# Kernel optimization log

Hardware: AMD Instinct MI355X
Metric: run time of the kernel (lower is better)

Reference implementation:

```python
import jax, jax.numpy as jnp
import numpy as np

HIDDEN = 1024
BATCH = 32
SRC_LEN = 2048
NEG_BIG = -1e10


def setup_inputs() -> dict:
    key = jax.random.key(0)
    k1, k2, k3, k4, k5, k6 = jax.random.split(key, 6)
    s = 1.0 / np.sqrt(2 * HIDDEN)
    return {
        "decoder_hidden": jax.random.normal(k1, (BATCH, HIDDEN), dtype=jnp.float32),
        "encoder_outputs": jax.random.normal(k2, (BATCH, SRC_LEN, HIDDEN), dtype=jnp.float32),
        "mask": jax.random.randint(k3, (BATCH, SRC_LEN), 0, 2, dtype=jnp.int32),
        # attn: Linear(2H -> H). Store as (2H, H) so x @ W matches torch x @ W.T
        "attn_W": jax.random.uniform(k4, (2 * HIDDEN, HIDDEN), jnp.float32, -s, s),
        "attn_b": jax.random.uniform(k5, (HIDDEN,), jnp.float32, -s, s),
        # v: Linear(H -> 1, bias=False), stored as (H,)
        "v_w": jax.random.uniform(k6, (HIDDEN,), jnp.float32, -1.0 / np.sqrt(HIDDEN), 1.0 / np.sqrt(HIDDEN)),
    }


def reference(decoder_hidden, encoder_outputs, mask, attn_W, attn_b, v_w):
    # Split the concat-linear: [dec, enc] @ W == dec @ W_dec + enc @ W_enc (same math, no big concat)
    W_dec, W_enc = attn_W[:HIDDEN], attn_W[HIDDEN:]
    dec_proj = decoder_hidden @ W_dec + attn_b            # (B, H)
    enc_proj = jnp.einsum("bsh,hk->bsk", encoder_outputs, W_enc)  # (B, S, H)
    energy = jnp.tanh(dec_proj[:, None, :] + enc_proj)    # (B, S, H)
    attention = jnp.einsum("bsh,h->bs", energy, v_w)      # (B, S)
    attention = jnp.where(mask == 0, NEG_BIG, attention)
    attention_weights = jax.nn.softmax(attention, axis=1)  # (B, S)
    context = jnp.einsum("bs,bsh->bh", attention_weights, encoder_outputs)  # (B, H)
    return attention_weights, context
```

## Files before the change

### kernel.cpp

```cpp
#include <hip/hip_runtime.h>
#include <hip/hip_bf16.h>
#include <math.h>

#define HIDDEN 1024
#define BATCH 32
#define SRC_LEN 2048
#define NROWS (BATCH * SRC_LEN)
#define NEG_BIG -10000000000.0f

typedef __attribute__((ext_vector_type(8))) short bf16x8;
typedef __attribute__((ext_vector_type(4))) float f32x4;
typedef __attribute__((ext_vector_type(4))) unsigned uint32x4;

static __device__ __forceinline__ unsigned short f2bf(float f) {
  unsigned u = __float_as_uint(f);
  u = u + 0x7fffu + ((u >> 16) & 1u);
  return (unsigned short)(u >> 16);
}

static __device__ __forceinline__ unsigned cvtpk(float lo, float hi) {
  unsigned r;
  asm("v_cvt_pk_bf16_f32 %0, %1, %2" : "=v"(r) : "v"(lo), "v"(hi));
  return r;
}

static __device__ __forceinline__ void gload16(const void* g, void* l) {
  __builtin_amdgcn_global_load_lds(
      reinterpret_cast<const __attribute__((address_space(1))) unsigned*>(
          reinterpret_cast<unsigned long long>(g)),
      reinterpret_cast<__attribute__((address_space(3))) unsigned*>(
          reinterpret_cast<unsigned long long>(l)),
      16, 0, 0);
}

__global__ __launch_bounds__(256) void k_wt(
    const float* __restrict__ W, unsigned short* __restrict__ WT) {
  __shared__ float ts[64][65];
  const int hy = blockIdx.y * 64, nx = blockIdx.x * 64;
  const int tid = threadIdx.x;
#pragma unroll
  for (int i = 0; i < 16; ++i) {
    int idx = tid + i * 256, r = idx >> 6, c = idx & 63;
    ts[r][c] = W[(HIDDEN + hy + r) * HIDDEN + nx + c];
  }
  __syncthreads();
#pragma unroll
  for (int i = 0; i < 16; ++i) {
    int idx = tid + i * 256, rn = idx >> 6, ch = idx & 63;
    WT[(nx + rn) * HIDDEN + hy + ch] = f2bf(ts[ch][rn]);
  }
}

__global__ __launch_bounds__(256) void k_dec_part(
    const float* __restrict__ dh, const float* __restrict__ W,
    float* __restrict__ decpart) {
  const int kl = threadIdx.x & 63;
  const int bq = threadIdx.x >> 6;
  const int k = blockIdx.x * 64 + kl;
  const int h0 = blockIdx.y * 64;
  __shared__ float dh_s[64][33];
#pragma unroll
  for (int i = 0; i < 8; ++i) {
    int idx = threadIdx.x + i * 256;
    int b = idx >> 6, hh = idx & 63;
    dh_s[hh][b] = dh[b * HIDDEN + h0 + hh];
  }
  __syncthreads();
  float acc[8] = {0.f, 0.f, 0.f, 0.f, 0.f, 0.f, 0.f, 0.f};
#pragma unroll
  for (int hh = 0; hh < 64; ++hh) {
    float w = W[(h0 + hh) * HIDDEN + k];
#pragma unroll
    for (int bb = 0; bb < 8; ++bb) acc[bb] += dh_s[hh][bq * 8 + bb] * w;
  }
#pragma unroll
  for (int bb = 0; bb < 8; ++bb)
    decpart[blockIdx.y * (BATCH * HIDDEN) + (bq * 8 + bb) * HIDDEN + k] = acc[bb];
}

__global__ __launch_bounds__(256) void k_dec_reduce(
    const float* __restrict__ decpart, const float* __restrict__ bias,
    float* __restrict__ out) {
  int e = blockIdx.x * 256 + threadIdx.x;
  float s = bias[e & (HIDDEN - 1)];
#pragma unroll
  for (int hc = 0; hc < 16; ++hc) s += decpart[hc * (BATCH * HIDDEN) + e];
  out[e] = s;
}

#define BM 256
#define BN 256
#define BK 64
#define NT (HIDDEN / BK)

__global__ __launch_bounds__(512, 2) void k_energy_mfma(
    const float* __restrict__ enc, const unsigned short* __restrict__ WT,
    const float* __restrict__ dec_proj, const float* __restrict__ v_w,
    float* __restrict__ part) {
  __shared__ unsigned short As[2][BM * BK];
  __shared__ unsigned short Bs[2][BN * BK];
  __shared__ float red[4][BM];

  const int tid = threadIdx.x;
  const int lane = tid & 63;
  const int wid = tid >> 6;
  const int wm = wid >> 2;
  const int wn = wid & 3;
  const int l16 = lane & 15;
  const int kg = lane >> 4;

  const int bid = blockIdx.x;
  const int l = (bid & 7) * 128 + (bid >> 3);
  const int n0 = (l & 3) * BN;
  const int row0 = (l >> 2) * BM;
  const int b = row0 >> 11;

  f32x4 acc[8][4];
#pragma unroll
  for (int m = 0; m < 8; ++m)
#pragma unroll
    for (int n = 0; n < 4; ++n) acc[m][n] = (f32x4){0.f, 0.f, 0.f, 0.f};

  const float4* enc4 = (const float4*)enc;

  const int rbase = tid >> 3;
  const int c16 = tid & 7;
  const float4* ea = enc4 + (size_t)(row0 + rbase) * 256 + c16 * 2;
  const unsigned aswz = ((unsigned)(rbase & 7)) << 4;
  const unsigned awoff = (unsigned)rbase * 128 + (((unsigned)c16 * 16) ^ aswz);

  const char* wb = (const char*)WT +
                   (size_t)(n0 + wid * 8 + (lane >> 3)) * 2048 +
                   ((((unsigned)(lane & 7)) * 16) ^ (((unsigned)(lane >> 3)) << 4));
  const unsigned bldsoff = (unsigned)wid * 1024;

  float4 pa[4][2];

#define STAGE_ISSUE(tile, pdst)                                            \
  do {                                                                     \
    _Pragma("unroll") for (int i = 0; i < 4; ++i)                          \
        gload16(wb + (size_t)i * 131072 + (size_t)(tile) * 128,            \
                (char*)Bs[pdst] + bldsoff + i * 8192);                     \
    _Pragma("unroll") for (int i = 0; i < 4; ++i) {                        \
      pa[i][0] = ea[(size_t)i * 16384 + (tile) * 16];                      \
      pa[i][1] = ea[(size_t)i * 16384 + (tile) * 16 + 1];                  \
    }                                                                      \
  } while (0)

#define STAGE_WRITE(pdst)                                                  \
  do {                                                                     \
    _Pragma("unroll") for (int i = 0; i < 4; ++i) {                        \
      uint32x4 q;                                                          \
      q.x = cvtpk(pa[i][0].x, pa[i][0].y);                                 \
      q.y = cvtpk(pa[i][0].z, pa[i][0].w);                                 \
      q.z = cvtpk(pa[i][1].x, pa[i][1].y);                                 \
      q.w = cvtpk(pa[i][1].z, pa[i][1].w);                                 \
      *(uint32x4*)((char*)As[pdst] + awoff + i * 8192) = q;                \
    }                                                                      \
  } while (0)

#define MFMA_STEP(p)                                                       \
  do {                                                                     \
    __builtin_amdgcn_s_setprio(1);                                         \
    _Pragma("unroll") for (int ks = 0; ks < 2; ++ks) {                     \
      bf16x8 af[8], bv[4];                                                 \
      _Pragma("unroll") for (int m = 0; m < 8; ++m) {                      \
        int r = wm * 128 + m * 16 + l16;                                   \
        unsigned off = (unsigned)r * 128 +                                 \
                       (((unsigned)(ks * 64 + kg * 16)) ^                  \
                        (((unsigned)(r & 7)) << 4));                       \
        af[m] = *(const bf16x8*)((const char*)As[p] + off);                \
      }                                                                    \
      _Pragma("unroll") for (int n = 0; n < 4; ++n) {                      \
        int c = wn * 64 + n * 16 + l16;                                    \
        unsigned off = (unsigned)c * 128 +                                 \
                       (((unsigned)(ks * 64 + kg * 16)) ^                  \
                        (((unsigned)(c & 7)) << 4));                       \
        bv[n] = *(const bf16x8*)((const char*)Bs[p] + off);                \
      }                                                                    \
      _Pragma("unroll") for (int m = 0; m < 8; ++m)                        \
          _Pragma("unroll") for (int n = 0; n < 4; ++n)                    \
              acc[m][n] = __builtin_amdgcn_mfma_f32_16x16x32_bf16(         \
                  af[m], bv[n], acc[m][n], 0, 0, 0);                       \
    }                                                                      \
    __builtin_amdgcn_s_setprio(0);                                         \
  } while (0)

#define STEP(tt, p)                                                        \
  do {                                                                     \
    if ((tt) + 1 < NT) STAGE_ISSUE((tt) + 1, (p) ^ 1);                     \
    MFMA_STEP(p);                                                          \
    if ((tt) + 1 < NT) STAGE_WRITE((p) ^ 1);                               \
    __syncthreads();                                                       \
  } while (0)

  STAGE_ISSUE(0, 0);
  STAGE_WRITE(0);
  __syncthreads();

  for (int t = 0; t < NT; t += 2) {
    STEP(t, 0);
    STEP(t + 1, 1);
  }

  float dv[4], vv[4];
#pragma unroll
  for (int n = 0; n < 4; ++n) {
    int kc = n0 + wn * 64 + n * 16 + l16;
    dv[n] = dec_proj[b * HIDDEN + kc];
    vv[n] = v_w[kc];
  }
#pragma unroll
  for (int m = 0; m < 8; ++m) {
#pragma unroll
    for (int r = 0; r < 4; ++r) {
      float p = 0.f;
#pragma unroll
      for (int n = 0; n < 4; ++n) {
        float x = dv[n] + acc[m][n][r];
        float t = 1.f - 2.f / (__expf(2.f * x) + 1.f);
        p += t * vv[n];
      }
      p += __shfl_xor(p, 1);
      p += __shfl_xor(p, 2);
      p += __shfl_xor(p, 4);
      p += __shfl_xor(p, 8);
      if (l16 == 0) red[wn][wm * 128 + m * 16 + kg * 4 + r] = p;
    }
  }
  __syncthreads();
  if (tid < BM) {
    float s = red[0][tid] + red[1][tid] + red[2][tid] + red[3][tid];
    part[(size_t)(l & 3) * NROWS + row0 + tid] = s;
  }
#undef STAGE_ISSUE
#undef STAGE_WRITE
#undef MFMA_STEP
#undef STEP
}

__global__ __launch_bounds__(256) void k_softmax(
    const float* __restrict__ part, const int* __restrict__ mask,
    float* __restrict__ out_w) {
  int b = blockIdx.x, tid = threadIdx.x;
  __shared__ float red[4], red2[4];
  float l[8];
  float m = -INFINITY;
#pragma unroll
  for (int j = 0; j < 8; ++j) {
    int s = tid + 256 * j;
    int row = b * SRC_LEN + s;
    float x = part[row] + part[NROWS + row] + part[2 * NROWS + row] +
              part[3 * NROWS + row];
    l[j] = (mask[row] == 0) ? NEG_BIG : x;
    m = fmaxf(m, l[j]);
  }
#pragma unroll
  for (int off = 32; off; off >>= 1) m = fmaxf(m, __shfl_xor(m, off));
  if ((tid & 63) == 0) red[tid >> 6] = m;
  __syncthreads();
  m = fmaxf(fmaxf(red[0], red[1]), fmaxf(red[2], red[3]));
  float sum = 0.f;
#pragma unroll
  for (int j = 0; j < 8; ++j) {
    l[j] = expf(l[j] - m);
    sum += l[j];
  }
#pragma unroll
  for (int off = 32; off; off >>= 1) sum += __shfl_xor(sum, off);
  if ((tid & 63) == 0) red2[tid >> 6] = sum;
  __syncthreads();
  sum = red2[0] + red2[1] + red2[2] + red2[3];
  float inv = 1.f / sum;
#pragma unroll
  for (int j = 0; j < 8; ++j) out_w[b * SRC_LEN + tid + 256 * j] = l[j] * inv;
}

__global__ __launch_bounds__(256) void k_ctx_partial(
    const float* __restrict__ w, const float* __restrict__ enc,
    float* __restrict__ part) {
  int b = blockIdx.x, sg = blockIdx.y, tid = threadIdx.x;
  const float4* enc4 = (const float4*)enc;
  float4 acc = {0.f, 0.f, 0.f, 0.f};
  int s0 = sg * 128;
#pragma unroll 4
  for (int s = 0; s < 128; ++s) {
    float ws = w[b * SRC_LEN + s0 + s];
    float4 e = enc4[(size_t)(b * SRC_LEN + s0 + s) * 256 + tid];
    acc.x += ws * e.x;
    acc.y += ws * e.y;
    acc.z += ws * e.z;
    acc.w += ws * e.w;
  }
  ((float4*)part)[(b * 16 + sg) * 256 + tid] = acc;
}

__global__ __launch_bounds__(256) void k_ctx_reduce(
    const float* __restrict__ part, float* __restrict__ ctx) {
  int b = blockIdx.x, tid = threadIdx.x;
  float4 acc = {0.f, 0.f, 0.f, 0.f};
#pragma unroll
  for (int sg = 0; sg < 16; ++sg) {
    float4 p = ((const float4*)part)[(b * 16 + sg) * 256 + tid];
    acc.x += p.x;
    acc.y += p.y;
    acc.z += p.z;
    acc.w += p.w;
  }
  ((float4*)ctx)[b * 256 + tid] = acc;
}

extern "C" void kernel_launch(void* const* d_in, const int* in_sizes, int n_in,
                              void* d_out, int out_size, void* d_ws, size_t ws_size,
                              hipStream_t stream) {
  const float* dh = (const float*)d_in[0];
  const float* enc = (const float*)d_in[1];
  const int* mask = (const int*)d_in[2];
  const float* attn_W = (const float*)d_in[3];
  const float* attn_b = (const float*)d_in[4];
  const float* v_w = (const float*)d_in[5];

  float* out_w = (float*)d_out;
  float* out_ctx = (float*)d_out + NROWS;

  float* ws = (float*)d_ws;
  float* part = ws;
  float* dec_proj = ws + 4 * NROWS;
  float* ctxpart = dec_proj + BATCH * HIDDEN;
  float* decpart = ctxpart + BATCH * 16 * HIDDEN;
  unsigned short* WT = (unsigned short*)(decpart + 16 * BATCH * HIDDEN);

  k_wt<<<dim3(16, 16), 256, 0, stream>>>(attn_W, WT);
  k_dec_part<<<dim3(16, 16), 256, 0, stream>>>(dh, attn_W, decpart);
  k_dec_reduce<<<dim3(128), 256, 0, stream>>>(decpart, attn_b, dec_proj);
  k_energy_mfma<<<dim3(1024), 512, 0, stream>>>(enc, WT, dec_proj, v_w, part);
  k_softmax<<<dim3(BATCH), 256, 0, stream>>>(part, mask, out_w);
  k_ctx_partial<<<dim3(BATCH, 16), 256, 0, stream>>>(out_w, enc, ctxpart);
  k_ctx_reduce<<<dim3(BATCH), 256, 0, stream>>>(ctxpart, out_ctx);
}
```

Baseline: 228.9 us.

## Split K-tile into four barrier-separated MFMA quads interleaved with loads

Result: slower. 258.6 us (+13.0%).

```diff
diff --git a/kernel.cpp b/kernel.cpp
--- a/kernel.cpp
+++ b/kernel.cpp
@@ -136,18 +136,22 @@
 
   float4 pa[4][2];
 
-#define STAGE_ISSUE(tile, pdst)                                            \
-  do {                                                                     \
-    _Pragma("unroll") for (int i = 0; i < 4; ++i)                          \
-        gload16(wb + (size_t)i * 131072 + (size_t)(tile) * 128,            \
-                (char*)Bs[pdst] + bldsoff + i * 8192);                     \
+#define ISSUE_A(tile)                                                      \
+  do {                                                                     \
     _Pragma("unroll") for (int i = 0; i < 4; ++i) {                        \
       pa[i][0] = ea[(size_t)i * 16384 + (tile) * 16];                      \
       pa[i][1] = ea[(size_t)i * 16384 + (tile) * 16 + 1];                  \
     }                                                                      \
   } while (0)
 
-#define STAGE_WRITE(pdst)                                                  \
+#define ISSUE_B(tile, pdst)                                                \
+  do {                                                                     \
+    _Pragma("unroll") for (int i = 0; i < 4; ++i)                          \
+        gload16(wb + (size_t)i * 131072 + (size_t)(tile) * 128,            \
+                (char*)Bs[pdst] + bldsoff + i * 8192);                     \
+  } while (0)
+
+#define CVT_WRITE_A(pdst)                                                  \
   do {                                                                     \
     _Pragma("unroll") for (int i = 0; i < 4; ++i) {                        \
       uint32x4 q;                                                          \
@@ -159,48 +163,82 @@
     }                                                                      \
   } while (0)
 
-#define MFMA_STEP(p)                                                       \
+#define DS_READ_A(p, mh, ks, af)                                           \
+  do {                                                                     \
+    _Pragma("unroll") for (int m = 0; m < 4; ++m) {                        \
+      int r = wm * 128 + (mh) * 64 + m * 16 + l16;                         \
+      unsigned off = (unsigned)r * 128 +                                   \
+          (((unsigned)((ks) * 64 + kg * 16)) ^ (((unsigned)(r & 7)) << 4));\
+      af[m] = *(const bf16x8*)((const char*)As[p] + off);                  \
+    }                                                                      \
+  } while (0)
+
+#define DS_READ_B(p, ks, bv)                                               \
+  do {                                                                     \
+    _Pragma("unroll") for (int n = 0; n < 4; ++n) {                        \
+      int c = wn * 64 + n * 16 + l16;                                      \
+      unsigned off = (unsigned)c * 128 +                                   \
+          (((unsigned)((ks) * 64 + kg * 16)) ^ (((unsigned)(c & 7)) << 4));\
+      bv[n] = *(const bf16x8*)((const char*)Bs[p] + off);                  \
+    }                                                                      \
+  } while (0)
+
+#define QUAD(mh, af, bv)                                                   \
   do {                                                                     \
     __builtin_amdgcn_s_setprio(1);                                         \
-    _Pragma("unroll") for (int ks = 0; ks < 2; ++ks) {                     \
-      bf16x8 af[8], bv[4];                                                 \
-      _Pragma("unroll") for (int m = 0; m < 8; ++m) {                      \
-        int r = wm * 128 + m * 16 + l16;                                   \
-        unsigned off = (unsigned)r * 128 +                                 \
-                       (((unsigned)(ks * 64 + kg * 16)) ^                  \
-                        (((unsigned)(r & 7)) << 4));                       \
-        af[m] = *(const bf16x8*)((const char*)As[p] + off);                \
-      }                                                                    \
-      _Pragma("unroll") for (int n = 0; n < 4; ++n) {                      \
-        int c = wn * 64 + n * 16 + l16;                                    \
-        unsigned off = (unsigned)c * 128 +                                 \
-                       (((unsigned)(ks * 64 + kg * 16)) ^                  \
-                        (((unsigned)(c & 7)) << 4));                       \
-        bv[n] = *(const bf16x8*)((const char*)Bs[p] + off);                \
-      }                                                                    \
-      _Pragma("unroll") for (int m = 0; m < 8; ++m)                        \
-          _Pragma("unroll") for (int n = 0; n < 4; ++n)                    \
-              acc[m][n] = __builtin_amdgcn_mfma_f32_16x16x32_bf16(         \
-                  af[m], bv[n], acc[m][n], 0, 0, 0);                       \
-    }                                                                      \
+    _Pragma("unroll") for (int m = 0; m < 4; ++m)                          \
+        _Pragma("unroll") for (int n = 0; n < 4; ++n)                      \
+            acc[(mh) * 4 + m][n] = __builtin_amdgcn_mfma_f32_16x16x32_bf16(\
+                af[m], bv[n], acc[(mh) * 4 + m][n], 0, 0, 0);              \
     __builtin_amdgcn_s_setprio(0);                                         \
   } while (0)
 
-#define STEP(tt, p)                                                        \
-  do {                                                                     \
-    if ((tt) + 1 < NT) STAGE_ISSUE((tt) + 1, (p) ^ 1);                     \
-    MFMA_STEP(p);                                                          \
-    if ((tt) + 1 < NT) STAGE_WRITE((p) ^ 1);                               \
-    __syncthreads();                                                       \
-  } while (0)
-
-  STAGE_ISSUE(0, 0);
-  STAGE_WRITE(0);
-  __syncthreads();
+#define LGKM0 asm volatile("s_waitcnt lgkmcnt(0)" ::: "memory")
+#define VM0 asm volatile("s_waitcnt vmcnt(0)" ::: "memory")
+#define BAR __builtin_amdgcn_s_barrier()
+#define SCHEDB __builtin_amdgcn_sched_barrier(0)
+
+#define KTILE(t, p)                                                        \
+  do {                                                                     \
+    bf16x8 af[4], bv[4];                                                   \
+                                                    \
+    DS_READ_A(p, 0, 0, af);                                                \
+    DS_READ_B(p, 0, bv);                                                   \
+    if ((t) + 1 < NT) ISSUE_A((t) + 1);                                    \
+    BAR; LGKM0; SCHEDB;                                                    \
+    QUAD(0, af, bv);                                                       \
+    BAR;                                                                   \
+                                         \
+    DS_READ_A(p, 1, 0, af);                                                \
+    if ((t) + 1 < NT) ISSUE_B((t) + 1, (p) ^ 1);                           \
+    BAR; LGKM0; SCHEDB;                                                    \
+    QUAD(1, af, bv);                                                       \
+    BAR;                                                                   \
+                                                    \
+    DS_READ_A(p, 0, 1, af);                                                \
+    DS_READ_B(p, 1, bv);                                                   \
+    BAR; LGKM0; SCHEDB;                                                    \
+    QUAD(0, af, bv);                                                       \
+    BAR;                                                                   \
+       \
+    DS_READ_A(p, 1, 1, af);                                                \
+    if ((t) + 1 < NT) CVT_WRITE_A((p) ^ 1);                                \
+    BAR; LGKM0; SCHEDB;                                                    \
+    QUAD(1, af, bv);                                                       \
+    if ((t) + 1 < NT) VM0;        \
+    BAR;                                 \
+  } while (0)
+
+  ISSUE_A(0);
+  ISSUE_B(0, 0);
+  CVT_WRITE_A(0);
+  VM0;
+  LGKM0;
+  BAR;
 
   for (int t = 0; t < NT; t += 2) {
-    STEP(t, 0);
-    STEP(t + 1, 1);
+    KTILE(t, 0);
+    KTILE(t + 1, 1);
   }
 
   float dv[4], vv[4];
@@ -233,10 +271,13 @@
     float s = red[0][tid] + red[1][tid] + red[2][tid] + red[3][tid];
     part[(size_t)(l & 3) * NROWS + row0 + tid] = s;
   }
-#undef STAGE_ISSUE
-#undef STAGE_WRITE
-#undef MFMA_STEP
-#undef STEP
+#undef ISSUE_A
+#undef ISSUE_B
+#undef CVT_WRITE_A
+#undef DS_READ_A
+#undef DS_READ_B
+#undef QUAD
+#undef KTILE
 }
 
 __global__ __launch_bounds__(256) void k_softmax(
```

## Shrink energy GEMM tiles to 128x128 with 256-thread blocks and 8-way column split

Applied to the files above, without the earlier changes.

Result: slower. 396.4 us (+73.2%).

```diff
diff --git a/kernel.cpp b/kernel.cpp
--- a/kernel.cpp
+++ b/kernel.cpp
@@ -88,102 +88,101 @@
   out[e] = s;
 }
 
-#define BM 256
-#define BN 256
+#define BM 128
+#define BN 128
 #define BK 64
 #define NT (HIDDEN / BK)
-
-__global__ __launch_bounds__(512, 2) void k_energy_mfma(
+#define NQ (HIDDEN / BN)
+
+__global__ __launch_bounds__(256, 2) void k_energy_mfma(
     const float* __restrict__ enc, const unsigned short* __restrict__ WT,
     const float* __restrict__ dec_proj, const float* __restrict__ v_w,
     float* __restrict__ part) {
   __shared__ unsigned short As[2][BM * BK];
   __shared__ unsigned short Bs[2][BN * BK];
-  __shared__ float red[4][BM];
+  __shared__ float red[2][BM];
 
   const int tid = threadIdx.x;
   const int lane = tid & 63;
   const int wid = tid >> 6;
-  const int wm = wid >> 2;
-  const int wn = wid & 3;
+  const int wm = wid >> 1;
+  const int wn = wid & 1;
   const int l16 = lane & 15;
   const int kg = lane >> 4;
 
   const int bid = blockIdx.x;
-  const int l = (bid & 7) * 128 + (bid >> 3);
-  const int n0 = (l & 3) * BN;
-  const int row0 = (l >> 2) * BM;
+  const int l = (bid & 7) * 512 + (bid >> 3);
+  const int n0 = (l & 7) * BN;
+  const int row0 = (l >> 3) * BM;
   const int b = row0 >> 11;
 
-  f32x4 acc[8][4];
-#pragma unroll
-  for (int m = 0; m < 8; ++m)
+  f32x4 acc[4][4];
+#pragma unroll
+  for (int m = 0; m < 4; ++m)
 #pragma unroll
     for (int n = 0; n < 4; ++n) acc[m][n] = (f32x4){0.f, 0.f, 0.f, 0.f};
 
   const float4* enc4 = (const float4*)enc;
 
-  const int rbase = tid >> 3;
-  const int c16 = tid & 7;
-  const float4* ea = enc4 + (size_t)(row0 + rbase) * 256 + c16 * 2;
+  const int rbase = tid >> 1;
+  const int hhalf = tid & 1;
+  const float4* ea = enc4 + (size_t)(row0 + rbase) * 256 + hhalf * 8;
   const unsigned aswz = ((unsigned)(rbase & 7)) << 4;
-  const unsigned awoff = (unsigned)rbase * 128 + (((unsigned)c16 * 16) ^ aswz);
+  const unsigned awoff = (unsigned)rbase * 128;
 
   const char* wb = (const char*)WT +
-                   (size_t)(n0 + wid * 8 + (lane >> 3)) * 2048 +
+                   (size_t)(n0 + wid * 32 + (lane >> 3)) * 2048 +
                    ((((unsigned)(lane & 7)) * 16) ^ (((unsigned)(lane >> 3)) << 4));
-  const unsigned bldsoff = (unsigned)wid * 1024;
-
-  float4 pa[4][2];
+  const unsigned bldsoff = (unsigned)wid * 4096;
+
+  float4 pa[8];
 
 #define STAGE_ISSUE(tile, pdst)                                            \
   do {                                                                     \
+    _Pragma("unroll") for (int j = 0; j < 8; ++j)                          \
+        pa[j] = ea[(size_t)(tile) * 16 + j];                               \
     _Pragma("unroll") for (int i = 0; i < 4; ++i)                          \
-        gload16(wb + (size_t)i * 131072 + (size_t)(tile) * 128,            \
-                (char*)Bs[pdst] + bldsoff + i * 8192);                     \
-    _Pragma("unroll") for (int i = 0; i < 4; ++i) {                        \
-      pa[i][0] = ea[(size_t)i * 16384 + (tile) * 16];                      \
-      pa[i][1] = ea[(size_t)i * 16384 + (tile) * 16 + 1];                  \
+        gload16(wb + (size_t)i * 16384 + (size_t)(tile) * 128,             \
+                (char*)Bs[pdst] + bldsoff + i * 1024);                     \
+  } while (0)
+
+#define STAGE_WRITE(pdst)                                                  \
+  do {                                                                     \
+    _Pragma("unroll") for (int j = 0; j < 4; ++j) {                        \
+      uint32x4 q;                                                          \
+      q.x = cvtpk(pa[2 * j].x, pa[2 * j].y);                               \
+      q.y = cvtpk(pa[2 * j].z, pa[2 * j].w);                               \
+      q.z = cvtpk(pa[2 * j + 1].x, pa[2 * j + 1].y);                       \
+      q.w = cvtpk(pa[2 * j + 1].z, pa[2 * j + 1].w);                       \
+      unsigned slot = (unsigned)(hhalf * 4 + j);                           \
+      *(uint32x4*)((char*)As[pdst] + awoff + ((slot * 16) ^ aswz)) = q;    \
     }                                                                      \
   } while (0)
 
-#define STAGE_WRITE(pdst)                                                  \
-  do {                                                                     \
-    _Pragma("unroll") for (int i = 0; i < 4; ++i) {                        \
-      uint32x4 q;                                                          \
-      q.x = cvtpk(pa[i][0].x, pa[i][0].y);                                 \
-      q.y = cvtpk(pa[i][0].z, pa[i][0].w);                                 \
-      q.z = cvtpk(pa[i][1].x, pa[i][1].y);                                 \
-      q.w = cvtpk(pa[i][1].z, pa[i][1].w);                                 \
-      *(uint32x4*)((char*)As[pdst] + awoff + i * 8192) = q;                \
-    }                                                                      \
-  } while (0)
-
 #define MFMA_STEP(p)                                                       \
   do {                                                                     \
-    __builtin_amdgcn_s_setprio(1);                                         \
     _Pragma("unroll") for (int ks = 0; ks < 2; ++ks) {                     \
-      bf16x8 af[8], bv[4];                                                 \
-      _Pragma("unroll") for (int m = 0; m < 8; ++m) {                      \
-        int r = wm * 128 + m * 16 + l16;                                   \
+      bf16x8 af[4], bv[4];                                                 \
+      const unsigned koff = (unsigned)(ks * 64 + kg * 16);                 \
+      _Pragma("unroll") for (int m = 0; m < 4; ++m) {                      \
+        int r = wm * 64 + m * 16 + l16;                                    \
         unsigned off = (unsigned)r * 128 +                                 \
-                       (((unsigned)(ks * 64 + kg * 16)) ^                  \
-                        (((unsigned)(r & 7)) << 4));                       \
+                       (koff ^ (((unsigned)(r & 7)) << 4));                \
         af[m] = *(const bf16x8*)((const char*)As[p] + off);                \
       }                                                                    \
       _Pragma("unroll") for (int n = 0; n < 4; ++n) {                      \
         int c = wn * 64 + n * 16 + l16;                                    \
         unsigned off = (unsigned)c * 128 +                                 \
-                       (((unsigned)(ks * 64 + kg * 16)) ^                  \
-                        (((unsigned)(c & 7)) << 4));                       \
+                       (koff ^ (((unsigned)(c & 7)) << 4));                \
         bv[n] = *(const bf16x8*)((const char*)Bs[p] + off);                \
       }                                                                    \
-      _Pragma("unroll") for (int m = 0; m < 8; ++m)                        \
+      __builtin_amdgcn_s_setprio(1);                                       \
+      _Pragma("unroll") for (int m = 0; m < 4; ++m)                        \
           _Pragma("unroll") for (int n = 0; n < 4; ++n)                    \
               acc[m][n] = __builtin_amdgcn_mfma_f32_16x16x32_bf16(         \
                   af[m], bv[n], acc[m][n], 0, 0, 0);                       \
+      __builtin_amdgcn_s_setprio(0);                                       \
     }                                                                      \
-    __builtin_amdgcn_s_setprio(0);                                         \
   } while (0)
 
 #define STEP(tt, p)                                                        \
@@ -211,7 +210,7 @@
     vv[n] = v_w[kc];
   }
 #pragma unroll
-  for (int m = 0; m < 8; ++m) {
+  for (int m = 0; m < 4; ++m) {
 #pragma unroll
     for (int r = 0; r < 4; ++r) {
       float p = 0.f;
@@ -225,13 +224,13 @@
       p += __shfl_xor(p, 2);
       p += __shfl_xor(p, 4);
       p += __shfl_xor(p, 8);
-      if (l16 == 0) red[wn][wm * 128 + m * 16 + kg * 4 + r] = p;
+      if (l16 == 0) red[wn][wm * 64 + m * 16 + kg * 4 + r] = p;
     }
   }
   __syncthreads();
   if (tid < BM) {
-    float s = red[0][tid] + red[1][tid] + red[2][tid] + red[3][tid];
-    part[(size_t)(l & 3) * NROWS + row0 + tid] = s;
+    float s = red[0][tid] + red[1][tid];
+    part[(size_t)(l & 7) * NROWS + row0 + tid] = s;
   }
 #undef STAGE_ISSUE
 #undef STAGE_WRITE
@@ -250,8 +249,9 @@
   for (int j = 0; j < 8; ++j) {
     int s = tid + 256 * j;
     int row = b * SRC_LEN + s;
-    float x = part[row] + part[NROWS + row] + part[2 * NROWS + row] +
-              part[3 * NROWS + row];
+    float x = 0.f;
+#pragma unroll
+    for (int q = 0; q < 8; ++q) x += part[(size_t)q * NROWS + row];
     l[j] = (mask[row] == 0) ? NEG_BIG : x;
     m = fmaxf(m, l[j]);
   }
@@ -325,15 +325,15 @@
 
   float* ws = (float*)d_ws;
   float* part = ws;
-  float* dec_proj = ws + 4 * NROWS;
-  float* ctxpart = dec_proj + BATCH * HIDDEN;
-  float* decpart = ctxpart + BATCH * 16 * HIDDEN;
-  unsigned short* WT = (unsigned short*)(decpart + 16 * BATCH * HIDDEN);
+  float* decpart = ws;
+  float* dec_proj = ws + 8 * NROWS;
+  unsigned short* WT = (unsigned short*)(dec_proj + BATCH * HIDDEN);
+  float* ctxpart = dec_proj + BATCH * HIDDEN + (HIDDEN * HIDDEN / 2);
 
   k_wt<<<dim3(16, 16), 256, 0, stream>>>(attn_W, WT);
   k_dec_part<<<dim3(16, 16), 256, 0, stream>>>(dh, attn_W, decpart);
   k_dec_reduce<<<dim3(128), 256, 0, stream>>>(decpart, attn_b, dec_proj);
-  k_energy_mfma<<<dim3(1024), 512, 0, stream>>>(enc, WT, dec_proj, v_w, part);
+  k_energy_mfma<<<dim3(4096), 256, 0, stream>>>(enc, WT, dec_proj, v_w, part);
   k_softmax<<<dim3(BATCH), 256, 0, stream>>>(part, mask, out_w);
   k_ctx_partial<<<dim3(BATCH, 16), 256, 0, stream>>>(out_w, enc, ctxpart);
   k_ctx_reduce<<<dim3(BATCH), 256, 0, stream>>>(ctxpart, out_ctx);
```
